# Kernel tuning notes

Measured on AMD Instinct MI355X. Metric: run time of the kernel, lower is better.

Reference implementation:

```python
import jax, jax.numpy as jnp
import numpy as np

T, B, D, H = 1024, 4, 1024, 16
HD = D // H  # 64


def _layernorm(x, g, b, eps=1e-5):
    mu = jnp.mean(x, axis=-1, keepdims=True)
    var = jnp.var(x, axis=-1, keepdims=True)
    return (x - mu) / jnp.sqrt(var + eps) * g + b


def setup_inputs() -> dict:
    key = jax.random.key(0)
    ks = jax.random.split(key, 16)
    s = 1.0 / np.sqrt(D)
    mk = lambda k: jax.random.uniform(k, (D, D), jnp.float32, -s, s)
    return {
        "x": jax.random.normal(ks[0], (T, B, D), jnp.float32),
        "Wq": mk(ks[1]), "bq": jnp.zeros((D,), jnp.float32),
        "Wk": mk(ks[2]), "bk": jnp.zeros((D,), jnp.float32),
        "Wv": mk(ks[3]), "bv": jnp.zeros((D,), jnp.float32),
        "Wo": mk(ks[4]), "bo": jnp.zeros((D,), jnp.float32),
        "Wl": mk(ks[5]), "bl": jnp.zeros((D,), jnp.float32),
        "g1": jnp.ones((D,), jnp.float32), "b1": jnp.zeros((D,), jnp.float32),
        "g2": jnp.ones((D,), jnp.float32), "b2": jnp.zeros((D,), jnp.float32),
    }


def reference(x, Wq, bq, Wk, bk, Wv, bv, Wo, bo, Wl, bl, g1, b1, g2, b2):
    # x: [T, B, D] (time-major). The torch loop over dim 0 with full keys/values
    # is equivalent to batched full (non-causal) self-attention.
    q = (x @ Wq.T + bq).reshape(T, B, H, HD)
    k = (x @ Wk.T + bk).reshape(T, B, H, HD)
    v = (x @ Wv.T + bv).reshape(T, B, H, HD)
    scores = jnp.einsum("tbhd,sbhd->bhts", q, k) / np.sqrt(HD).astype(np.float32)
    attn = jax.nn.softmax(scores, axis=-1)          # [B,H,T,T]
    ctx = jnp.einsum("bhts,sbhd->tbhd", attn, v).reshape(T, B, D)
    attn_out = ctx @ Wo.T + bo
    # dropout p: identity at inference
    h = _layernorm(attn_out + x, g1, b1)
    ffn = h @ Wl.T + bl
    return _layernorm(ffn + h, g2, b2)
```

## Files before the change

### kernel.cpp

```cpp
#include <hip/hip_runtime.h>

#define T_ 1024
#define B_ 4
#define D_ 1024
#define H_ 16
#define HD_ 64
#define M_ (T_ * B_)

typedef _Float16 f16;
typedef f16 f16x8 __attribute__((ext_vector_type(8)));
typedef f16 f16x4 __attribute__((ext_vector_type(4)));
typedef float f32x4 __attribute__((ext_vector_type(4)));

__device__ __forceinline__ void gl2lds16(const void* g, void* l) {
  __builtin_amdgcn_global_load_lds(
      (const __attribute__((address_space(1))) void*)g,
      (__attribute__((address_space(3))) void*)l, 16, 0, 0);
}

__global__ __launch_bounds__(256) void cvt_f32_f16(const float* __restrict__ in,
                                                   f16* __restrict__ out, int n) {
  int i = (blockIdx.x * 256 + threadIdx.x) * 4;
  if (i >= n) return;
  float4 v = *(const float4*)(in + i);
  f16x4 o = {(f16)v.x, (f16)v.y, (f16)v.z, (f16)v.w};
  *(f16x4*)(out + i) = o;
}

struct WPtrs {
  const float* s[5];
  f16* d[5];
};

__global__ __launch_bounds__(256) void cvt5(WPtrs p) {
  const int a = blockIdx.x >> 10;
  const int i = ((blockIdx.x & 1023) * 256 + threadIdx.x) * 4;
  float4 v = *(const float4*)(p.s[a] + i);
  f16x4 o = {(f16)v.x, (f16)v.y, (f16)v.z, (f16)v.w};
  *(f16x4*)(p.d[a] + i) = o;
}

__global__ __launch_bounds__(256) void bcat(const float* __restrict__ b0,
                                            const float* __restrict__ b1,
                                            const float* __restrict__ b2,
                                            float* __restrict__ dst) {
  const float* src = blockIdx.x == 0 ? b0 : (blockIdx.x == 1 ? b1 : b2);
  const int i = threadIdx.x * 4;
  *(float4*)(dst + blockIdx.x * 1024 + i) = *(const float4*)(src + i);
}

__global__ __launch_bounds__(256) void gemm_f16(const f16* __restrict__ A,
                                                const f16* __restrict__ W,
                                                const float* __restrict__ bias,
                                                const float* __restrict__ res,
                                                float* __restrict__ out) {
  constexpr int K = D_, BK = 32;
  __shared__ __align__(16) f16 As[128 * BK];
  __shared__ __align__(16) f16 Bs[64 * BK];
  const int tid = threadIdx.x;
  const int lane = tid & 63;
  const int quad = lane >> 4, l16 = lane & 15;
  const int m0 = blockIdx.y * 128, n0 = blockIdx.x * 64;
  const int wave = tid >> 6;
  const int wm = (wave >> 1) * 64, wn = (wave & 1) * 32;
  f32x4 acc[4][2] = {};
  for (int kt = 0; kt < K / BK; ++kt) {
    __syncthreads();
    const int kb = kt * BK;
#pragma unroll
    for (int i = 0; i < 2; ++i) {
      const int c = i * 256 + tid;
      const int row = c >> 2, col8 = (c & 3) * 8;
      const int ldsbase = (i * 256 + (tid & ~63)) * 8;
      gl2lds16(A + (size_t)(m0 + row) * K + kb + col8, &As[ldsbase]);
    }
    {
      const int row = tid >> 2, col8 = (tid & 3) * 8;
      const int ldsbase = (tid & ~63) * 8;
      gl2lds16(W + (size_t)(n0 + row) * K + kb + col8, &Bs[ldsbase]);
    }
    __syncthreads();
    f16x8 af[4], bf[2];
#pragma unroll
    for (int i = 0; i < 4; ++i)
      af[i] = *(const f16x8*)&As[(wm + i * 16 + l16) * BK + quad * 8];
#pragma unroll
    for (int j = 0; j < 2; ++j)
      bf[j] = *(const f16x8*)&Bs[(wn + j * 16 + l16) * BK + quad * 8];
#pragma unroll
    for (int i = 0; i < 4; ++i)
#pragma unroll
      for (int j = 0; j < 2; ++j)
        acc[i][j] = __builtin_amdgcn_mfma_f32_16x16x32_f16(af[i], bf[j], acc[i][j], 0, 0, 0);
  }
#pragma unroll
  for (int j = 0; j < 2; ++j) {
    const int n = n0 + wn + j * 16 + l16;
    const float bn = bias[n];
#pragma unroll
    for (int i = 0; i < 4; ++i) {
      const int m = m0 + wm + i * 16 + quad * 4;
#pragma unroll
      for (int r = 0; r < 4; ++r)
        out[(size_t)(m + r) * D_ + n] = acc[i][j][r] + bn + res[(size_t)(m + r) * D_ + n];
    }
  }
}

#define QSCALE 0.18033688011112042f
__global__ __launch_bounds__(256) void gemm_qkv(const f16* __restrict__ A,
                                                const f16* __restrict__ W,
                                                const float* __restrict__ bias,
                                                f16* __restrict__ qo,
                                                f16* __restrict__ ko,
                                                f16* __restrict__ vo) {
  constexpr int K = D_, BK = 32;
  __shared__ __align__(16) f16 As[128 * BK];
  __shared__ __align__(16) f16 Bs[128 * BK];
  const int tid = threadIdx.x;
  const int lane = tid & 63;
  const int quad = lane >> 4, l16 = lane & 15;
  const int m0 = blockIdx.y * 128, n0 = blockIdx.x * 128;
  const int wave = tid >> 6;
  const int wm = (wave >> 1) * 64, wn = (wave & 1) * 64;
  f32x4 acc[4][4] = {};
  for (int kt = 0; kt < K / BK; ++kt) {
    __syncthreads();
    const int kb = kt * BK;
#pragma unroll
    for (int i = 0; i < 2; ++i) {
      const int c = i * 256 + tid;
      const int row = c >> 2, col8 = (c & 3) * 8;
      const int ldsbase = (i * 256 + (tid & ~63)) * 8;
      gl2lds16(A + (size_t)(m0 + row) * K + kb + col8, &As[ldsbase]);
      gl2lds16(W + (size_t)(n0 + row) * K + kb + col8, &Bs[ldsbase]);
    }
    __syncthreads();
    f16x8 af[4], bf[4];
#pragma unroll
    for (int i = 0; i < 4; ++i)
      af[i] = *(const f16x8*)&As[(wm + i * 16 + l16) * BK + quad * 8];
#pragma unroll
    for (int j = 0; j < 4; ++j)
      bf[j] = *(const f16x8*)&Bs[(wn + j * 16 + l16) * BK + quad * 8];
#pragma unroll
    for (int i = 0; i < 4; ++i)
#pragma unroll
      for (int j = 0; j < 4; ++j)
        acc[i][j] = __builtin_amdgcn_mfma_f32_16x16x32_f16(af[i], bf[j], acc[i][j], 0, 0, 0);
  }
  const int which = n0 >> 10;
  f16* outp = which == 0 ? qo : (which == 1 ? ko : vo);
  const float sc = which == 0 ? QSCALE : 1.0f;
#pragma unroll
  for (int j = 0; j < 4; ++j) {
    const int n = n0 + wn + j * 16 + l16;
    const float bn = bias[n];
    const int nl = n & 1023;
    const int hh = nl >> 6, d = nl & 63;
#pragma unroll
    for (int i = 0; i < 4; ++i) {
#pragma unroll
      for (int r = 0; r < 4; ++r) {
        const int m = m0 + wm + i * 16 + quad * 4 + r;
        const float v = (acc[i][j][r] + bn) * sc;
        const int t = m >> 2, bb = m & 3;
        if (which < 2)
          outp[((size_t)(bb * H_ + hh) * T_ + t) * HD_ + d] = (f16)v;
        else
          outp[((size_t)(bb * H_ + hh) * HD_ + d) * T_ + t] = (f16)v;
      }
    }
  }
}

__global__ __launch_bounds__(256) void attn(const f16* __restrict__ Q,
                                            const f16* __restrict__ Km,
                                            const f16* __restrict__ Vt,
                                            f16* __restrict__ ctx) {
  constexpr int SK = 128;
  constexpr int NT = T_ / SK;
  __shared__ __align__(16) f16 Ks[SK * HD_];
  __shared__ __align__(16) f16 Vs[HD_ * SK];
  __shared__ __align__(16) f16 Ps[4][16 * 36];
  const int tid = threadIdx.x, wave = tid >> 6, lane = tid & 63;
  const int quad = lane >> 4, l16 = lane & 15;
  const int b = blockIdx.z, h = blockIdx.y, q0 = blockIdx.x * 128;
  const f16* Qbh = Q + ((size_t)(b * H_ + h) * T_ + q0 + wave * 32) * HD_;
  const f16* Kbh = Km + (size_t)(b * H_ + h) * T_ * HD_;
  const f16* Vbh = Vt + (size_t)(b * H_ + h) * HD_ * T_;

  f16x8 qf[2][2];
#pragma unroll
  for (int c = 0; c < 2; ++c) {
    qf[c][0] = *(const f16x8*)&Qbh[(c * 16 + l16) * HD_ + quad * 8];
    qf[c][1] = *(const f16x8*)&Qbh[(c * 16 + l16) * HD_ + 32 + quad * 8];
  }

  const f16* kq[4];
  const f16* vq[4];
  int lds_o[4];
#pragma unroll
  for (int it = 0; it < 4; ++it) {
    const int n = wave * 256 + it * 64 + lane;
    const int s = n >> 3, cp = n & 7, cl = cp ^ (s & 7);
    kq[it] = Kbh + (size_t)s * HD_ + cl * 8;
    const int d = n >> 4, cp2 = n & 15, cl2 = cp2 ^ (d & 7);
    vq[it] = Vbh + (size_t)d * T_ + cl2 * 8;
    lds_o[it] = (wave * 256 + it * 64) * 8;
  }

  f32x4 O[4][2] = {};
  float lsum[2] = {0.f, 0.f};
  const int sw = l16 & 7;

  for (int kt = 0; kt < NT; ++kt) {
    __syncthreads();
#pragma unroll
    for (int it = 0; it < 4; ++it) {
      gl2lds16(kq[it], &Ks[lds_o[it]]);
      kq[it] += SK * HD_;
    }
#pragma unroll
    for (int it = 0; it < 4; ++it) {
      gl2lds16(vq[it], &Vs[lds_o[it]]);
      vq[it] += SK;
    }
    __syncthreads();

    float st[8][2][4];
#pragma unroll
    for (int s = 0; s < 8; ++s) {
      const int row = s * 16 + l16;
      const f16x8 ka = *(const f16x8*)&Ks[row * HD_ + (quad ^ sw) * 8];
      const f16x8 kb = *(const f16x8*)&Ks[row * HD_ + ((4 + quad) ^ sw) * 8];
#pragma unroll
      for (int c = 0; c < 2; ++c) {
        f32x4 a = {};
        a = __builtin_amdgcn_mfma_f32_16x16x32_f16(ka, qf[c][0], a, 0, 0, 0);
        a = __builtin_amdgcn_mfma_f32_16x16x32_f16(kb, qf[c][1], a, 0, 0, 0);
#pragma unroll
        for (int r = 0; r < 4; ++r) {
          st[s][c][r] = exp2f(a[r]);
          lsum[c] += st[s][c][r];
        }
      }
    }

#pragma unroll
    for (int cI = 0; cI < 4; ++cI) {
#pragma unroll
      for (int c = 0; c < 2; ++c) {
        f16* pw = &Ps[wave][0];
        f16x4 w0, w1;
#pragma unroll
        for (int r = 0; r < 4; ++r) {
          w0[r] = (f16)st[2 * cI][c][r];
          w1[r] = (f16)st[2 * cI + 1][c][r];
        }
        *(f16x4*)&pw[l16 * 36 + quad * 4] = w0;
        *(f16x4*)&pw[l16 * 36 + 16 + quad * 4] = w1;
        const f16x8 pf = *(const f16x8*)&pw[l16 * 36 + quad * 8];
#pragma unroll
        for (int dt = 0; dt < 4; ++dt) {
          const int d = dt * 16 + l16;
          const f16x8 vf = *(const f16x8*)&Vs[d * SK + (((cI * 4 + quad) ^ sw) * 8)];
          O[dt][c] = __builtin_amdgcn_mfma_f32_16x16x32_f16(vf, pf, O[dt][c], 0, 0, 0);
        }
      }
    }
  }

#pragma unroll
  for (int c = 0; c < 2; ++c) {
    float l = lsum[c];
    l += __shfl_xor(l, 16, 64);
    l += __shfl_xor(l, 32, 64);
    const float linv = 1.f / l;
    const int t = q0 + wave * 32 + c * 16 + l16;
#pragma unroll
    for (int dt = 0; dt < 4; ++dt) {
      f16x4 ov;
#pragma unroll
      for (int r = 0; r < 4; ++r) ov[r] = (f16)(O[dt][c][r] * linv);
      *(f16x4*)&ctx[((size_t)t * B_ + b) * D_ + h * HD_ + dt * 16 + quad * 4] = ov;
    }
  }
}

__global__ __launch_bounds__(256) void lnorm(const float* __restrict__ a,
                                             const float* __restrict__ g,
                                             const float* __restrict__ bb,
                                             float* __restrict__ out,
                                             f16* __restrict__ outh) {
  const int row = blockIdx.x, tid = threadIdx.x;
  const size_t base = (size_t)row * D_;
  float4 va = *(const float4*)&a[base + tid * 4];
  float x0 = va.x, x1 = va.y, x2 = va.z, x3 = va.w;
  float s = x0 + x1 + x2 + x3;
  float sq = x0 * x0 + x1 * x1 + x2 * x2 + x3 * x3;
#pragma unroll
  for (int off = 32; off; off >>= 1) {
    s += __shfl_down(s, off, 64);
    sq += __shfl_down(sq, off, 64);
  }
  __shared__ float rs[4], rq[4];
  __shared__ float mean_s, rstd_s;
  if ((tid & 63) == 0) { rs[tid >> 6] = s; rq[tid >> 6] = sq; }
  __syncthreads();
  if (tid == 0) {
    float S = rs[0] + rs[1] + rs[2] + rs[3];
    float Qq = rq[0] + rq[1] + rq[2] + rq[3];
    float mean = S / D_;
    float var = Qq / D_ - mean * mean;
    mean_s = mean;
    rstd_s = rsqrtf(var + 1e-5f);
  }
  __syncthreads();
  const float mean = mean_s, rstd = rstd_s;
  float4 vg = *(const float4*)&g[tid * 4];
  float4 vb = *(const float4*)&bb[tid * 4];
  float y0 = (x0 - mean) * rstd * vg.x + vb.x;
  float y1 = (x1 - mean) * rstd * vg.y + vb.y;
  float y2 = (x2 - mean) * rstd * vg.z + vb.z;
  float y3 = (x3 - mean) * rstd * vg.w + vb.w;
  *(float4*)&out[base + tid * 4] = make_float4(y0, y1, y2, y3);
  if (outh) {
    f16x4 o = {(f16)y0, (f16)y1, (f16)y2, (f16)y3};
    *(f16x4*)&outh[base + tid * 4] = o;
  }
}

extern "C" void kernel_launch(void* const* d_in, const int* in_sizes, int n_in,
                              void* d_out, int out_size, void* d_ws, size_t ws_size,
                              hipStream_t stream) {
  const float* x  = (const float*)d_in[0];
  const float* Wq = (const float*)d_in[1];
  const float* bq = (const float*)d_in[2];
  const float* Wk = (const float*)d_in[3];
  const float* bk = (const float*)d_in[4];
  const float* Wv = (const float*)d_in[5];
  const float* bv = (const float*)d_in[6];
  const float* Wo = (const float*)d_in[7];
  const float* bo = (const float*)d_in[8];
  const float* Wl = (const float*)d_in[9];
  const float* bl = (const float*)d_in[10];
  const float* g1 = (const float*)d_in[11];
  const float* b1 = (const float*)d_in[12];
  const float* g2 = (const float*)d_in[13];
  const float* b2 = (const float*)d_in[14];

  char* ws = (char*)d_ws;
  const size_t MB = 1 << 20;
  f16*   xb   = (f16*)(ws + 0 * MB);
  f16*   wqkv = (f16*)(ws + 8 * MB);
  f16*   wob  = (f16*)(ws + 14 * MB);
  f16*   wlb  = (f16*)(ws + 16 * MB);
  float* bqkv = (float*)(ws + 18 * MB);
  f16*   qb   = (f16*)(ws + 19 * MB);
  f16*   kb   = (f16*)(ws + 27 * MB);
  f16*   vb   = (f16*)(ws + 35 * MB);
  f16*   ctxb = xb;
  float* att  = (float*)qb;
  f16*   hb   = vb;
  float* hbuf = (float*)ws;

  cvt_f32_f16<<<M_ * D_ / 1024, 256, 0, stream>>>(x, xb, M_ * D_);
  WPtrs wp;
  wp.s[0] = Wq; wp.s[1] = Wk; wp.s[2] = Wv; wp.s[3] = Wo; wp.s[4] = Wl;
  wp.d[0] = wqkv; wp.d[1] = wqkv + D_ * D_; wp.d[2] = wqkv + 2 * D_ * D_;
  wp.d[3] = wob; wp.d[4] = wlb;
  cvt5<<<5 * 1024, 256, 0, stream>>>(wp);
  bcat<<<3, 256, 0, stream>>>(bq, bk, bv, bqkv);

  gemm_qkv<<<dim3(3 * D_ / 128, M_ / 128), 256, 0, stream>>>(xb, wqkv, bqkv, qb, kb, vb);

  attn<<<dim3(T_ / 128, H_, B_), 256, 0, stream>>>(qb, kb, vb, ctxb);

  dim3 gg(D_ / 64, M_ / 128);
  gemm_f16<<<gg, 256, 0, stream>>>(ctxb, wob, bo, x, att);
  lnorm<<<M_, 256, 0, stream>>>(att, g1, b1, hbuf, hb);
  gemm_f16<<<gg, 256, 0, stream>>>(hb, wlb, bl, hbuf, att);
  lnorm<<<M_, 256, 0, stream>>>(att, g2, b2, (float*)d_out, nullptr);
}
```

Measured before the change: 255.0 us.

## Double GEMM K-tile to 64 with XOR-swizzled LDS and remap attention grid

Both GEMM kernels now stage a 64-wide K slice per iteration instead of 32. This halves the number of barrier-separated loop iterations, and an XOR swizzle on the 16-byte column chunks is meant to avoid LDS bank conflicts on the fragment reads. The attention launch is remapped so blockIdx.x walks batch-head pairs and blockIdx.y walks query tiles, which changes block scheduling order and the L2 locality of K/V. LDS use per block doubles, which may reduce occupancy.

```diff
diff --git a/kernel.cpp b/kernel.cpp
--- a/kernel.cpp
+++ b/kernel.cpp
@@ -49,12 +49,13 @@
   *(float4*)(dst + blockIdx.x * 1024 + i) = *(const float4*)(src + i);
 }
 
+
 __global__ __launch_bounds__(256) void gemm_f16(const f16* __restrict__ A,
                                                 const f16* __restrict__ W,
                                                 const float* __restrict__ bias,
                                                 const float* __restrict__ res,
                                                 float* __restrict__ out) {
-  constexpr int K = D_, BK = 32;
+  constexpr int K = D_, BK = 64;
   __shared__ __align__(16) f16 As[128 * BK];
   __shared__ __align__(16) f16 Bs[64 * BK];
   const int tid = threadIdx.x;
@@ -68,30 +69,39 @@
     __syncthreads();
     const int kb = kt * BK;
 #pragma unroll
+    for (int i = 0; i < 4; ++i) {
+      const int c = i * 256 + tid;
+      const int row = c >> 3, p = c & 7, g = p ^ (row & 7);
+      gl2lds16(A + (size_t)(m0 + row) * K + kb + g * 8,
+               &As[(i * 256 + (tid & ~63)) * 8]);
+    }
+#pragma unroll
     for (int i = 0; i < 2; ++i) {
       const int c = i * 256 + tid;
-      const int row = c >> 2, col8 = (c & 3) * 8;
-      const int ldsbase = (i * 256 + (tid & ~63)) * 8;
-      gl2lds16(A + (size_t)(m0 + row) * K + kb + col8, &As[ldsbase]);
-    }
-    {
-      const int row = tid >> 2, col8 = (tid & 3) * 8;
-      const int ldsbase = (tid & ~63) * 8;
-      gl2lds16(W + (size_t)(n0 + row) * K + kb + col8, &Bs[ldsbase]);
-    }
-    __syncthreads();
-    f16x8 af[4], bf[2];
-#pragma unroll
-    for (int i = 0; i < 4; ++i)
-      af[i] = *(const f16x8*)&As[(wm + i * 16 + l16) * BK + quad * 8];
-#pragma unroll
-    for (int j = 0; j < 2; ++j)
-      bf[j] = *(const f16x8*)&Bs[(wn + j * 16 + l16) * BK + quad * 8];
-#pragma unroll
-    for (int i = 0; i < 4; ++i)
-#pragma unroll
-      for (int j = 0; j < 2; ++j)
-        acc[i][j] = __builtin_amdgcn_mfma_f32_16x16x32_f16(af[i], bf[j], acc[i][j], 0, 0, 0);
+      const int row = c >> 3, p = c & 7, g = p ^ (row & 7);
+      gl2lds16(W + (size_t)(n0 + row) * K + kb + g * 8,
+               &Bs[(i * 256 + (tid & ~63)) * 8]);
+    }
+    __syncthreads();
+#pragma unroll
+    for (int h = 0; h < 2; ++h) {
+      f16x8 af[4], bf[2];
+#pragma unroll
+      for (int i = 0; i < 4; ++i) {
+        const int r = wm + i * 16 + l16;
+        af[i] = *(const f16x8*)&As[r * 64 + (((h * 4 + quad) ^ (r & 7)) * 8)];
+      }
+#pragma unroll
+      for (int j = 0; j < 2; ++j) {
+        const int r = wn + j * 16 + l16;
+        bf[j] = *(const f16x8*)&Bs[r * 64 + (((h * 4 + quad) ^ (r & 7)) * 8)];
+      }
+#pragma unroll
+      for (int i = 0; i < 4; ++i)
+#pragma unroll
+        for (int j = 0; j < 2; ++j)
+          acc[i][j] = __builtin_amdgcn_mfma_f32_16x16x32_f16(af[i], bf[j], acc[i][j], 0, 0, 0);
+    }
   }
 #pragma unroll
   for (int j = 0; j < 2; ++j) {
@@ -114,7 +124,7 @@
                                                 f16* __restrict__ qo,
                                                 f16* __restrict__ ko,
                                                 f16* __restrict__ vo) {
-  constexpr int K = D_, BK = 32;
+  constexpr int K = D_, BK = 64;
   __shared__ __align__(16) f16 As[128 * BK];
   __shared__ __align__(16) f16 Bs[128 * BK];
   const int tid = threadIdx.x;
@@ -128,26 +138,33 @@
     __syncthreads();
     const int kb = kt * BK;
 #pragma unroll
-    for (int i = 0; i < 2; ++i) {
+    for (int i = 0; i < 4; ++i) {
       const int c = i * 256 + tid;
-      const int row = c >> 2, col8 = (c & 3) * 8;
-      const int ldsbase = (i * 256 + (tid & ~63)) * 8;
-      gl2lds16(A + (size_t)(m0 + row) * K + kb + col8, &As[ldsbase]);
-      gl2lds16(W + (size_t)(n0 + row) * K + kb + col8, &Bs[ldsbase]);
-    }
-    __syncthreads();
-    f16x8 af[4], bf[4];
-#pragma unroll
-    for (int i = 0; i < 4; ++i)
-      af[i] = *(const f16x8*)&As[(wm + i * 16 + l16) * BK + quad * 8];
-#pragma unroll
-    for (int j = 0; j < 4; ++j)
-      bf[j] = *(const f16x8*)&Bs[(wn + j * 16 + l16) * BK + quad * 8];
-#pragma unroll
-    for (int i = 0; i < 4; ++i)
-#pragma unroll
-      for (int j = 0; j < 4; ++j)
-        acc[i][j] = __builtin_amdgcn_mfma_f32_16x16x32_f16(af[i], bf[j], acc[i][j], 0, 0, 0);
+      const int row = c >> 3, p = c & 7, g = p ^ (row & 7);
+      const int ldsb = (i * 256 + (tid & ~63)) * 8;
+      gl2lds16(A + (size_t)(m0 + row) * K + kb + g * 8, &As[ldsb]);
+      gl2lds16(W + (size_t)(n0 + row) * K + kb + g * 8, &Bs[ldsb]);
+    }
+    __syncthreads();
+#pragma unroll
+    for (int h = 0; h < 2; ++h) {
+      f16x8 af[4], bf[4];
+#pragma unroll
+      for (int i = 0; i < 4; ++i) {
+        const int r = wm + i * 16 + l16;
+        af[i] = *(const f16x8*)&As[r * 64 + (((h * 4 + quad) ^ (r & 7)) * 8)];
+      }
+#pragma unroll
+      for (int j = 0; j < 4; ++j) {
+        const int r = wn + j * 16 + l16;
+        bf[j] = *(const f16x8*)&Bs[r * 64 + (((h * 4 + quad) ^ (r & 7)) * 8)];
+      }
+#pragma unroll
+      for (int i = 0; i < 4; ++i)
+#pragma unroll
+        for (int j = 0; j < 4; ++j)
+          acc[i][j] = __builtin_amdgcn_mfma_f32_16x16x32_f16(af[i], bf[j], acc[i][j], 0, 0, 0);
+    }
   }
   const int which = n0 >> 10;
   f16* outp = which == 0 ? qo : (which == 1 ? ko : vo);
@@ -185,10 +202,12 @@
   __shared__ __align__(16) f16 Ps[4][16 * 36];
   const int tid = threadIdx.x, wave = tid >> 6, lane = tid & 63;
   const int quad = lane >> 4, l16 = lane & 15;
-  const int b = blockIdx.z, h = blockIdx.y, q0 = blockIdx.x * 128;
-  const f16* Qbh = Q + ((size_t)(b * H_ + h) * T_ + q0 + wave * 32) * HD_;
-  const f16* Kbh = Km + (size_t)(b * H_ + h) * T_ * HD_;
-  const f16* Vbh = Vt + (size_t)(b * H_ + h) * HD_ * T_;
+  const int bh = blockIdx.x;
+  const int b = bh >> 4, h = bh & 15;
+  const int q0 = blockIdx.y * 128;
+  const f16* Qbh = Q + ((size_t)bh * T_ + q0 + wave * 32) * HD_;
+  const f16* Kbh = Km + (size_t)bh * T_ * HD_;
+  const f16* Vbh = Vt + (size_t)bh * HD_ * T_;
 
   f16x8 qf[2][2];
 #pragma unroll
@@ -375,7 +394,7 @@
 
   gemm_qkv<<<dim3(3 * D_ / 128, M_ / 128), 256, 0, stream>>>(xb, wqkv, bqkv, qb, kb, vb);
 
-  attn<<<dim3(T_ / 128, H_, B_), 256, 0, stream>>>(qb, kb, vb, ctxb);
+  attn<<<dim3(B_ * H_, T_ / 128), 256, 0, stream>>>(qb, kb, vb, ctxb);
 
   dim3 gg(D_ / 64, M_ / 128);
   gemm_f16<<<gg, 256, 0, stream>>>(ctxb, wob, bo, x, att);
```

Result: no change. 255.3 us (+0.1%).
